# Kernel optimization log

Measured on AMD Instinct MI355X. Metric: run time of the kernel, lower is better.

Reference implementation:

```python
import jax, jax.numpy as jnp
import numpy as np

# --- constants matching the torch module's default-camera / material / light setup ---
IMAGE_SIZE = 128
SCALE = 1.0
FOCAL = 12.0
R_MAT = jnp.array([[-1.0, 0.0, 0.0], [0.0, 1.0, 0.0], [0.0, 0.0, -1.0]], dtype=jnp.float32)
T_VEC = jnp.array([0.0, 0.0, 2.0 * SCALE], dtype=jnp.float32)
CAM_POS = jnp.array([0.0, 0.0, 2.0 * SCALE], dtype=jnp.float32)  # camera center in world coords
LIGHT_LOC = jnp.array([0.0, 1.0, 3.0], dtype=jnp.float32)
AMB_L, DIFF_L, SPEC_L = 0.5, 0.3, 0.2          # PointLights defaults
MAT_AMB, MAT_DIFF, MAT_SPEC = 1.0, 1.0, 0.6    # Materials(specular_color=0.6)
SHININESS = 10.0
TEXEL = jnp.array([142.0, 179.0, 247.0], dtype=jnp.float32) / 255.0  # uniform vertex color
BG = 1.0  # BlendParams background
EPS = 1e-8


def _normalize(v):
    return v / (jnp.linalg.norm(v, axis=-1, keepdims=True) + EPS)


def _render_one(verts, faces):
    """verts: [V,3] world space; faces: [F,3] int. Returns ([3,H,W] rgb*255, [1,H,W] alpha)."""
    H = W = IMAGE_SIZE
    # world -> view (PyTorch3D row-vector convention: x_view = x @ R + T)
    view = verts @ R_MAT + T_VEC              # [V,3]
    z = view[:, 2]                            # [V] view-space depth (>0 in front)
    ndc = FOCAL * view[:, :2] / z[:, None]    # [V,2] perspective projection to NDC
    tri = ndc[faces]                          # [F,3,2]
    tz = z[faces]                             # [F,3]

    # pixel centers in NDC (PyTorch3D: +x left, +y up)
    xs = 1.0 - (2.0 * jnp.arange(W) + 1.0) / W
    ys = 1.0 - (2.0 * jnp.arange(H) + 1.0) / H
    gy, gx = jnp.meshgrid(ys, xs, indexing='ij')
    px = gx.reshape(-1).astype(jnp.float32)   # [P]
    py = gy.reshape(-1).astype(jnp.float32)   # [P]

    v0, v1, v2 = tri[:, 0], tri[:, 1], tri[:, 2]   # [F,2]

    def edge(a, b):  # signed area cross(b-a, p-a) for all pixels -> [P,F]
        return ((b[:, 0] - a[:, 0])[None] * (py[:, None] - a[:, 1][None])
                - (b[:, 1] - a[:, 1])[None] * (px[:, None] - a[:, 0][None]))

    area = ((v1[:, 0] - v0[:, 0]) * (v2[:, 1] - v0[:, 1])
            - (v1[:, 1] - v0[:, 1]) * (v2[:, 0] - v0[:, 0]))   # [F]
    area_safe = jnp.where(jnp.abs(area) < EPS, EPS, area)
    b0 = edge(v1, v2) / area_safe             # [P,F]
    b1 = edge(v2, v0) / area_safe
    b2 = 1.0 - b0 - b1
    inside = (b0 >= 0) & (b1 >= 0) & (b2 >= 0) & (jnp.abs(area) > EPS)[None]

    # perspective-correct interpolated depth: z_pix = 1 / sum_i(b_i / z_i)
    S = b0 / tz[:, 0] + b1 / tz[:, 1] + b2 / tz[:, 2]
    depth = jnp.where(inside & (S > EPS), 1.0 / jnp.maximum(S, EPS), jnp.inf)
    fidx = jnp.argmin(depth, axis=1)          # [P] z-buffer winner (faces_per_pixel=1)
    hit = jnp.isfinite(jnp.min(depth, axis=1))

    # --- recompute barycentrics only for the winning face per pixel (cheap, [P]) ---
    f = faces[fidx]                           # [P,3]
    tv = ndc[f]                               # [P,3,2]
    tzp = z[f]                                # [P,3]
    a0, a1, a2 = tv[:, 0], tv[:, 1], tv[:, 2]

    def edge_p(a, b):
        return (b[:, 0] - a[:, 0]) * (py - a[:, 1]) - (b[:, 1] - a[:, 1]) * (px - a[:, 0])

    ar = (a1[:, 0] - a0[:, 0]) * (a2[:, 1] - a0[:, 1]) - (a1[:, 1] - a0[:, 1]) * (a2[:, 0] - a0[:, 0])
    ar = jnp.where(jnp.abs(ar) < EPS, EPS, ar)
    bb0 = edge_p(a1, a2) / ar
    bb1 = edge_p(a2, a0) / ar
    bb2 = 1.0 - bb0 - bb1
    w = jnp.stack([bb0 / tzp[:, 0], bb1 / tzp[:, 1], bb2 / tzp[:, 2]], axis=-1)
    pc = w / (jnp.sum(w, axis=-1, keepdims=True) + EPS)   # [P,3] perspective-correct barycentrics

    # --- vertex normals (world space) ---
    fv = verts[faces]                         # [F,3,3]
    fn = jnp.cross(fv[:, 1] - fv[:, 0], fv[:, 2] - fv[:, 0])  # [F,3]
    vn = (jnp.zeros_like(verts)
          .at[faces[:, 0]].add(fn)
          .at[faces[:, 1]].add(fn)
          .at[faces[:, 2]].add(fn))
    vn = _normalize(vn)

    # --- interpolate position/normal, Phong shade ---
    pos = jnp.einsum('pk,pkd->pd', pc, verts[f])   # [P,3]
    nrm = _normalize(jnp.einsum('pk,pkd->pd', pc, vn[f]))
    l = _normalize(LIGHT_LOC - pos)
    vdir = _normalize(CAM_POS - pos)
    ndl = jax.nn.relu(jnp.sum(nrm * l, axis=-1))          # [P]
    refl = 2.0 * jnp.sum(nrm * l, axis=-1, keepdims=True) * nrm - l
    spec_cos = jax.nn.relu(jnp.sum(refl * vdir, axis=-1))
    ambient = AMB_L * MAT_AMB
    diffuse = DIFF_L * MAT_DIFF * ndl
    specular = SPEC_L * MAT_SPEC * spec_cos ** SHININESS
    color = TEXEL[None] * (ambient + diffuse[:, None]) + specular[:, None]

    rgb = jnp.where(hit[:, None], color, BG)              # hard blend with white bg
    alpha = hit.astype(verts.dtype)
    img = rgb.reshape(H, W, 3).transpose(2, 0, 1) * 255.0  # [3,H,W]
    a = alpha.reshape(1, H, W)
    return img, a


def setup_inputs() -> dict:
    key = jax.random.key(0)
    k1, k2 = jax.random.split(key)
    B, V, F = 2, 1300, 2500
    vertices = jax.random.normal(k1, (B, V, 3), dtype=jnp.float32) * 0.05  # head-scale mesh near origin
    faces = jax.random.randint(k2, (F, 3), 0, V, dtype=jnp.int32)
    return {"vertices": vertices, "faces": faces}


def reference(vertices, faces):
    # ori_size == image_size, so the area-interpolation in the torch module is the identity.
    images, alphas = jax.lax.map(lambda v: _render_one(v, faces), vertices)
    return images, alphas
```

## Files before the change

### kernel.cpp

```cpp
#include <hip/hip_runtime.h>
#include <math.h>

#pragma clang fp contract(off)

#define IMG_H 128
#define IMG_W 128
#define HW (IMG_H * IMG_W)
#define NB 2
#define NV 1300
#define NF 2500
#define EPSF 1e-8f
#define NCHUNK 32
#define CHUNK ((NF + NCHUNK - 1) / NCHUNK)
#define NREG 128
#define NBLK (NREG * NB * NCHUNK)

#define OFF_FACE 31232
#define OFF_DBUF 351488

#define DINIT 0x7F800000FFFFFFFFull

__global__ __launch_bounds__(256) void k_face(const float* __restrict__ verts,
                                              const int* __restrict__ faces,
                                              float* __restrict__ vn,
                                              float4* __restrict__ face) {
    int i = blockIdx.x * 256 + threadIdx.x;
    if (i >= NB * NF) return;
    int b = i / NF;
    int f = i - b * NF;
    int i0 = faces[f * 3 + 0];
    int i1 = faces[f * 3 + 1];
    int i2 = faces[f * 3 + 2];
    const float* wv = verts + (size_t)b * NV * 3;
    float v0x = wv[i0 * 3 + 0], v0y = wv[i0 * 3 + 1], v0z = wv[i0 * 3 + 2];
    float v1x = wv[i1 * 3 + 0], v1y = wv[i1 * 3 + 1], v1z = wv[i1 * 3 + 2];
    float v2x = wv[i2 * 3 + 0], v2y = wv[i2 * 3 + 1], v2z = wv[i2 * 3 + 2];
    float z0 = 2.0f - v0z, z1 = 2.0f - v1z, z2 = 2.0f - v2z;
    float p0x = (12.0f * (-v0x)) / z0, p0y = (12.0f * v0y) / z0;
    float p1x = (12.0f * (-v1x)) / z1, p1y = (12.0f * v1y) / z1;
    float p2x = (12.0f * (-v2x)) / z2, p2y = (12.0f * v2y) / z2;

    float t1 = (p1x - p0x) * (p2y - p0y);
    float t2 = (p1y - p0y) * (p2x - p0x);
    float area = t1 - t2;
    float aabs = fabsf(area);
    float area_safe = (aabs < EPSF) ? EPSF : area;
    bool valid = aabs > EPSF;
    float minx, maxx, miny, maxy;
    if (valid) {
        minx = fminf(p0x, fminf(p1x, p2x)) - 1e-3f;
        maxx = fmaxf(p0x, fmaxf(p1x, p2x)) + 1e-3f;
        miny = fminf(p0y, fminf(p1y, p2y)) - 1e-3f;
        maxy = fmaxf(p0y, fmaxf(p1y, p2y)) + 1e-3f;
    } else {
        minx = 1e30f; maxx = -1e30f; miny = 1e30f; maxy = -1e30f;
    }
    int o = (b * NF + f) * 4;
    face[o + 0] = make_float4(p2x - p1x, p2y - p1y, p1x, p1y);
    face[o + 1] = make_float4(p0x - p2x, p0y - p2y, p2x, p2y);
    face[o + 2] = make_float4(area_safe, z0, z1, z2);
    face[o + 3] = make_float4(minx, maxx, miny, maxy);

    float ax = v1x - v0x, ay = v1y - v0y, az = v1z - v0z;
    float bx = v2x - v0x, by = v2y - v0y, bz = v2z - v0z;
    float fnx = ay * bz - az * by;
    float fny = az * bx - ax * bz;
    float fnz = ax * by - ay * bx;
    float* vnb = vn + (size_t)b * NV * 3;
    atomicAdd(&vnb[i0 * 3 + 0], fnx);
    atomicAdd(&vnb[i0 * 3 + 1], fny);
    atomicAdd(&vnb[i0 * 3 + 2], fnz);
    atomicAdd(&vnb[i1 * 3 + 0], fnx);
    atomicAdd(&vnb[i1 * 3 + 1], fny);
    atomicAdd(&vnb[i1 * 3 + 2], fnz);
    atomicAdd(&vnb[i2 * 3 + 0], fnx);
    atomicAdd(&vnb[i2 * 3 + 1], fny);
    atomicAdd(&vnb[i2 * 3 + 2], fnz);
}

__global__ __launch_bounds__(128) void k_raster(const float4* __restrict__ face,
                                                unsigned long long* __restrict__ dbuf) {
    __shared__ float4 sface[2][CHUNK * 4];
    __shared__ unsigned short sidx[2][CHUNK];

    int bx = blockIdx.x;
    int chunk = bx & (NCHUNK - 1);
    int tmp = bx >> 5;
    int b = tmp & 1;
    int reg = tmp >> 1;
    int r0 = (reg >> 3) * 8;
    int c0 = (reg & 7) * 16;
    int f0 = chunk * CHUNK;
    int nf = NF - f0; if (nf > CHUNK) nf = CHUNK;

    int t = threadIdx.x;
    int wid = t >> 6, lid = t & 63;
    int cw0 = c0 + wid * 8;

    float txhi = 1.0f - (2.0f * (float)cw0 + 1.0f) / 128.0f;
    float txlo = 1.0f - (2.0f * (float)(cw0 + 7) + 1.0f) / 128.0f;
    float tyhi = 1.0f - (2.0f * (float)r0 + 1.0f) / 128.0f;
    float tylo = 1.0f - (2.0f * (float)(r0 + 7) + 1.0f) / 128.0f;

    const float4* fb = face + (size_t)b * NF * 4;

    int cnt = 0;
    for (int base = 0; base < nf; base += 64) {
        int tt = base + lid;
        bool pass = false;
        float4 bb, E0, E1, FD;
        if (tt < nf) {
            bb = fb[(f0 + tt) * 4 + 3];
            pass = (bb.y >= txlo) && (bb.x <= txhi) && (bb.w >= tylo) && (bb.z <= tyhi);
            if (pass) {
                E0 = fb[(f0 + tt) * 4 + 0];
                E1 = fb[(f0 + tt) * 4 + 1];
                FD = fb[(f0 + tt) * 4 + 2];
                float as = FD.x;
                float u0l = E0.x * (tylo - E0.w), u0h = E0.x * (tyhi - E0.w);
                float u0mn = fminf(u0l, u0h), u0mx = fmaxf(u0l, u0h);
                float u1l = E1.x * (tylo - E1.w), u1h = E1.x * (tyhi - E1.w);
                float u1mn = fminf(u1l, u1h), u1mx = fmaxf(u1l, u1h);
                float v0l = E0.y * (txlo - E0.z), v0h = E0.y * (txhi - E0.z);
                float v0mn = fminf(v0l, v0h), v0mx = fmaxf(v0l, v0h);
                float v1l = E1.y * (txlo - E1.z), v1h = E1.y * (txhi - E1.z);
                float v1mn = fminf(v1l, v1h), v1mx = fmaxf(v1l, v1h);
                float e0mx = u0mx - v0mn, e0mn = u0mn - v0mx;
                float e1mx = u1mx - v1mn, e1mn = u1mn - v1mx;
                const float DL = 1e-4f;
                bool ok;
                if (as > 0.0f) {
                    ok = (e0mx >= -DL) && (e1mx >= -DL) && (((as - e0mn) - e1mn) >= -DL);
                } else {
                    ok = (e0mn <= DL) && (e1mn <= DL) && (((as - e0mx) - e1mx) <= DL);
                }
                pass = ok;
            }
        }
        unsigned long long m = __ballot(pass);
        if (pass) {
            int pos = cnt + __popcll(m & ((1ull << lid) - 1ull));
            sface[wid][pos * 4 + 0] = E0;
            sface[wid][pos * 4 + 1] = E1;
            sface[wid][pos * 4 + 2] = FD;
            sface[wid][pos * 4 + 3] = bb;
            sidx[wid][pos] = (unsigned short)tt;
        }
        cnt += __popcll(m);
    }

    int r = r0 + (lid >> 3);
    int c = cw0 + (lid & 7);
    int p = r * IMG_W + c;
    float px = 1.0f - (2.0f * (float)c + 1.0f) / 128.0f;
    float py = 1.0f - (2.0f * (float)r + 1.0f) / 128.0f;

    unsigned long long best = DINIT;
    for (int j = 0; j < cnt; ++j) {
        float4 fbb = sface[wid][j * 4 + 3];
        if (px >= fbb.x && px <= fbb.y && py >= fbb.z && py <= fbb.w) {
            float4 e0v = sface[wid][j * 4 + 0];
            float4 e1v = sface[wid][j * 4 + 1];
            float4 fdv = sface[wid][j * 4 + 2];
            float u1 = e0v.x * (py - e0v.w);
            float u2 = e0v.y * (px - e0v.z);
            float e0 = u1 - u2;
            float u3 = e1v.x * (py - e1v.w);
            float u4 = e1v.y * (px - e1v.z);
            float e1 = u3 - u4;
            float as = fdv.x;
            bool ok = (as > 0.0f) ? (e0 >= 0.0f && e1 >= 0.0f)
                                  : (e0 <= 0.0f && e1 <= 0.0f);
            if (ok) {
                float b0 = e0 / as;
                float b1 = e1 / as;
                float b2 = (1.0f - b0) - b1;
                if (b2 >= 0.0f) {
                    float S = ((b0 / fdv.y) + (b1 / fdv.z)) + (b2 / fdv.w);
                    if (S > EPSF) {
                        float depth = 1.0f / fmaxf(S, EPSF);
                        unsigned long long pk =
                            ((unsigned long long)__float_as_uint(depth) << 32) |
                            (unsigned)(f0 + sidx[wid][j]);
                        if (pk < best) best = pk;
                    }
                }
            }
        }
    }
    dbuf[((size_t)chunk * NB + b) * HW + p] = best;
}

__global__ __launch_bounds__(64) void k_shade(const float* __restrict__ verts,
                                              const int* __restrict__ faces,
                                              const float* __restrict__ vn,
                                              const unsigned long long* __restrict__ dbuf,
                                              float* __restrict__ out) {
    int i = blockIdx.x * 64 + threadIdx.x;
    int b = i >> 14;
    int p = i & (HW - 1);
    unsigned long long pk = DINIT;
    for (int k = 0; k < NCHUNK; ++k) {
        unsigned long long v = dbuf[((size_t)k * NB + b) * HW + p];
        if (v < pk) pk = v;
    }
    unsigned dbits = (unsigned)(pk >> 32);
    bool hit = dbits < 0x7F800000u;
    float cr = 255.0f, cg = 255.0f, cb = 255.0f, alpha = 0.0f;
    if (hit) {
        alpha = 1.0f;
        int f = (int)(unsigned)(pk & 0xFFFFFFFFull);
        int row = p >> 7;
        int col = p & 127;
        float px = 1.0f - (2.0f * (float)col + 1.0f) / 128.0f;
        float py = 1.0f - (2.0f * (float)row + 1.0f) / 128.0f;
        int i0 = faces[f * 3 + 0];
        int i1 = faces[f * 3 + 1];
        int i2 = faces[f * 3 + 2];
        const float* wv = verts + (size_t)b * NV * 3;
        float v0x = wv[i0 * 3 + 0], v0y = wv[i0 * 3 + 1], v0z = wv[i0 * 3 + 2];
        float v1x = wv[i1 * 3 + 0], v1y = wv[i1 * 3 + 1], v1z = wv[i1 * 3 + 2];
        float v2x = wv[i2 * 3 + 0], v2y = wv[i2 * 3 + 1], v2z = wv[i2 * 3 + 2];
        float z0 = 2.0f - v0z, z1 = 2.0f - v1z, z2 = 2.0f - v2z;
        float a0x = (12.0f * (-v0x)) / z0, a0y = (12.0f * v0y) / z0;
        float a1x = (12.0f * (-v1x)) / z1, a1y = (12.0f * v1y) / z1;
        float a2x = (12.0f * (-v2x)) / z2, a2y = (12.0f * v2y) / z2;

        float t1 = (a1x - a0x) * (a2y - a0y);
        float t2 = (a1y - a0y) * (a2x - a0x);
        float ar = t1 - t2;
        ar = (fabsf(ar) < EPSF) ? EPSF : ar;
        float u1 = (a2x - a1x) * (py - a1y);
        float u2 = (a2y - a1y) * (px - a1x);
        float bb0 = (u1 - u2) / ar;
        float u3 = (a0x - a2x) * (py - a2y);
        float u4 = (a0y - a2y) * (px - a2x);
        float bb1 = (u3 - u4) / ar;
        float bb2 = (1.0f - bb0) - bb1;
        float w0 = bb0 / z0;
        float w1 = bb1 / z1;
        float w2 = bb2 / z2;
        float denom = ((w0 + w1) + w2) + EPSF;
        float pc0 = w0 / denom;
        float pc1 = w1 / denom;
        float pc2 = w2 / denom;

        float posx = (pc0 * v0x + pc1 * v1x) + pc2 * v2x;
        float posy = (pc0 * v0y + pc1 * v1y) + pc2 * v2y;
        float posz = (pc0 * v0z + pc1 * v1z) + pc2 * v2z;

        const float* vnb = vn + (size_t)b * NV * 3;
        float n0x = vnb[i0 * 3 + 0], n0y = vnb[i0 * 3 + 1], n0z = vnb[i0 * 3 + 2];
        float n1x = vnb[i1 * 3 + 0], n1y = vnb[i1 * 3 + 1], n1z = vnb[i1 * 3 + 2];
        float n2x = vnb[i2 * 3 + 0], n2y = vnb[i2 * 3 + 1], n2z = vnb[i2 * 3 + 2];
        float in0 = 1.0f / (sqrtf(n0x * n0x + n0y * n0y + n0z * n0z) + EPSF);
        float in1 = 1.0f / (sqrtf(n1x * n1x + n1y * n1y + n1z * n1z) + EPSF);
        float in2 = 1.0f / (sqrtf(n2x * n2x + n2y * n2y + n2z * n2z) + EPSF);
        n0x *= in0; n0y *= in0; n0z *= in0;
        n1x *= in1; n1y *= in1; n1z *= in1;
        n2x *= in2; n2y *= in2; n2z *= in2;
        float nx = (pc0 * n0x + pc1 * n1x) + pc2 * n2x;
        float ny = (pc0 * n0y + pc1 * n1y) + pc2 * n2y;
        float nz = (pc0 * n0z + pc1 * n1z) + pc2 * n2z;
        float inn = 1.0f / (sqrtf(nx * nx + ny * ny + nz * nz) + EPSF);
        nx *= inn; ny *= inn; nz *= inn;

        float lx = 0.0f - posx, ly = 1.0f - posy, lz = 3.0f - posz;
        float iln = 1.0f / (sqrtf(lx * lx + ly * ly + lz * lz) + EPSF);
        lx *= iln; ly *= iln; lz *= iln;
        float vx = 0.0f - posx, vy = 0.0f - posy, vz = 2.0f - posz;
        float ivn = 1.0f / (sqrtf(vx * vx + vy * vy + vz * vz) + EPSF);
        vx *= ivn; vy *= ivn; vz *= ivn;

        float ndl = nx * lx + ny * ly + nz * lz;
        float ndlr = fmaxf(ndl, 0.0f);
        float rx = 2.0f * ndl * nx - lx;
        float ry = 2.0f * ndl * ny - ly;
        float rz = 2.0f * ndl * nz - lz;
        float sc = fmaxf(rx * vx + ry * vy + rz * vz, 0.0f);
        float spec = 0.2f * 0.6f * powf(sc, 10.0f);
        float shade = 0.5f * 1.0f + 0.3f * 1.0f * ndlr;
        cr = ((142.0f / 255.0f) * shade + spec) * 255.0f;
        cg = ((179.0f / 255.0f) * shade + spec) * 255.0f;
        cb = ((247.0f / 255.0f) * shade + spec) * 255.0f;
    }
    float* img = out + (size_t)b * 3 * HW;
    img[0 * HW + p] = cr;
    img[1 * HW + p] = cg;
    img[2 * HW + p] = cb;
    out[(size_t)NB * 3 * HW + (size_t)b * HW + p] = alpha;
}

extern "C" void kernel_launch(void* const* d_in, const int* in_sizes, int n_in,
                              void* d_out, int out_size, void* d_ws, size_t ws_size,
                              hipStream_t stream) {
    const float* verts = (const float*)d_in[0];
    const int* faces = (const int*)d_in[1];
    char* ws = (char*)d_ws;
    float* vn = (float*)(ws + 0);
    float4* face = (float4*)(ws + OFF_FACE);
    unsigned long long* dbuf = (unsigned long long*)(ws + OFF_DBUF);
    float* out = (float*)d_out;

    hipMemsetAsync(vn, 0, NB * NV * 3 * sizeof(float), stream);
    k_face<<<(NB * NF + 255) / 256, 256, 0, stream>>>(verts, faces, vn, face);
    k_raster<<<NBLK, 128, 0, stream>>>(face, dbuf);
    k_shade<<<(NB * HW) / 64, 64, 0, stream>>>(verts, faces, vn, dbuf, out);
}
```

Before: 101.8 us.

## Use SoA face layout and readlane broadcast instead of LDS compaction in raster

Face records are stored structure-of-arrays so each of the four float4 fields is read with coalesced loads. The raster kernel no longer compacts surviving faces into shared memory and re-reads them. Instead it walks the ballot mask and broadcasts each surviving face's data from its lane with readlane, then tests all pixels against it. This removes the LDS traffic and the two-phase structure. In exchange all four float4s are now loaded unconditionally, and each survivor costs sixteen scalar readlanes.

Result: slower. 103.9 us (+2.1%).

```diff
diff --git a/kernel.cpp b/kernel.cpp
--- a/kernel.cpp
+++ b/kernel.cpp
@@ -19,6 +19,10 @@
 #define OFF_DBUF 351488
 
 #define DINIT 0x7F800000FFFFFFFFull
+
+__device__ __forceinline__ float bcastf(float v, int s) {
+    return __int_as_float(__builtin_amdgcn_readlane(__float_as_int(v), s));
+}
 
 __global__ __launch_bounds__(256) void k_face(const float* __restrict__ verts,
                                               const int* __restrict__ faces,
@@ -55,11 +59,11 @@
     } else {
         minx = 1e30f; maxx = -1e30f; miny = 1e30f; maxy = -1e30f;
     }
-    int o = (b * NF + f) * 4;
-    face[o + 0] = make_float4(p2x - p1x, p2y - p1y, p1x, p1y);
-    face[o + 1] = make_float4(p0x - p2x, p0y - p2y, p2x, p2y);
-    face[o + 2] = make_float4(area_safe, z0, z1, z2);
-    face[o + 3] = make_float4(minx, maxx, miny, maxy);
+    int o = b * NF + f;
+    face[0 * NB * NF + o] = make_float4(p2x - p1x, p2y - p1y, p1x, p1y);
+    face[1 * NB * NF + o] = make_float4(p0x - p2x, p0y - p2y, p2x, p2y);
+    face[2 * NB * NF + o] = make_float4(area_safe, z0, z1, z2);
+    face[3 * NB * NF + o] = make_float4(minx, maxx, miny, maxy);
 
     float ax = v1x - v0x, ay = v1y - v0y, az = v1z - v0z;
     float bx = v2x - v0x, by = v2y - v0y, bz = v2z - v0z;
@@ -80,9 +84,6 @@
 
 __global__ __launch_bounds__(128) void k_raster(const float4* __restrict__ face,
                                                 unsigned long long* __restrict__ dbuf) {
-    __shared__ float4 sface[2][CHUNK * 4];
-    __shared__ unsigned short sidx[2][CHUNK];
-
     int bx = blockIdx.x;
     int chunk = bx & (NCHUNK - 1);
     int tmp = bx >> 5;
@@ -102,20 +103,30 @@
     float tyhi = 1.0f - (2.0f * (float)r0 + 1.0f) / 128.0f;
     float tylo = 1.0f - (2.0f * (float)(r0 + 7) + 1.0f) / 128.0f;
 
-    const float4* fb = face + (size_t)b * NF * 4;
-
-    int cnt = 0;
+    const float4* pE0 = face + (size_t)(0 * NB + b) * NF + f0;
+    const float4* pE1 = face + (size_t)(1 * NB + b) * NF + f0;
+    const float4* pFD = face + (size_t)(2 * NB + b) * NF + f0;
+    const float4* pBB = face + (size_t)(3 * NB + b) * NF + f0;
+
+    int r = r0 + (lid >> 3);
+    int c = cw0 + (lid & 7);
+    int p = r * IMG_W + c;
+    float px = 1.0f - (2.0f * (float)c + 1.0f) / 128.0f;
+    float py = 1.0f - (2.0f * (float)r + 1.0f) / 128.0f;
+
+    unsigned long long best = DINIT;
+
     for (int base = 0; base < nf; base += 64) {
         int tt = base + lid;
+        int fi = (tt < nf) ? tt : (nf - 1);
+        float4 bb = pBB[fi];
+        float4 E0 = pE0[fi];
+        float4 E1 = pE1[fi];
+        float4 FD = pFD[fi];
         bool pass = false;
-        float4 bb, E0, E1, FD;
         if (tt < nf) {
-            bb = fb[(f0 + tt) * 4 + 3];
             pass = (bb.y >= txlo) && (bb.x <= txhi) && (bb.w >= tylo) && (bb.z <= tyhi);
             if (pass) {
-                E0 = fb[(f0 + tt) * 4 + 0];
-                E1 = fb[(f0 + tt) * 4 + 1];
-                FD = fb[(f0 + tt) * 4 + 2];
                 float as = FD.x;
                 float u0l = E0.x * (tylo - E0.w), u0h = E0.x * (tyhi - E0.w);
                 float u0mn = fminf(u0l, u0h), u0mx = fmaxf(u0l, u0h);
@@ -128,61 +139,47 @@
                 float e0mx = u0mx - v0mn, e0mn = u0mn - v0mx;
                 float e1mx = u1mx - v1mn, e1mn = u1mn - v1mx;
                 const float DL = 1e-4f;
-                bool ok;
                 if (as > 0.0f) {
-                    ok = (e0mx >= -DL) && (e1mx >= -DL) && (((as - e0mn) - e1mn) >= -DL);
+                    pass = (e0mx >= -DL) && (e1mx >= -DL) && (((as - e0mn) - e1mn) >= -DL);
                 } else {
-                    ok = (e0mn <= DL) && (e1mn <= DL) && (((as - e0mx) - e1mx) <= DL);
+                    pass = (e0mn <= DL) && (e1mn <= DL) && (((as - e0mx) - e1mx) <= DL);
                 }
-                pass = ok;
             }
         }
         unsigned long long m = __ballot(pass);
-        if (pass) {
-            int pos = cnt + __popcll(m & ((1ull << lid) - 1ull));
-            sface[wid][pos * 4 + 0] = E0;
-            sface[wid][pos * 4 + 1] = E1;
-            sface[wid][pos * 4 + 2] = FD;
-            sface[wid][pos * 4 + 3] = bb;
-            sidx[wid][pos] = (unsigned short)tt;
-        }
-        cnt += __popcll(m);
-    }
-
-    int r = r0 + (lid >> 3);
-    int c = cw0 + (lid & 7);
-    int p = r * IMG_W + c;
-    float px = 1.0f - (2.0f * (float)c + 1.0f) / 128.0f;
-    float py = 1.0f - (2.0f * (float)r + 1.0f) / 128.0f;
-
-    unsigned long long best = DINIT;
-    for (int j = 0; j < cnt; ++j) {
-        float4 fbb = sface[wid][j * 4 + 3];
-        if (px >= fbb.x && px <= fbb.y && py >= fbb.z && py <= fbb.w) {
-            float4 e0v = sface[wid][j * 4 + 0];
-            float4 e1v = sface[wid][j * 4 + 1];
-            float4 fdv = sface[wid][j * 4 + 2];
-            float u1 = e0v.x * (py - e0v.w);
-            float u2 = e0v.y * (px - e0v.z);
-            float e0 = u1 - u2;
-            float u3 = e1v.x * (py - e1v.w);
-            float u4 = e1v.y * (px - e1v.z);
-            float e1 = u3 - u4;
-            float as = fdv.x;
-            bool ok = (as > 0.0f) ? (e0 >= 0.0f && e1 >= 0.0f)
-                                  : (e0 <= 0.0f && e1 <= 0.0f);
-            if (ok) {
-                float b0 = e0 / as;
-                float b1 = e1 / as;
-                float b2 = (1.0f - b0) - b1;
-                if (b2 >= 0.0f) {
-                    float S = ((b0 / fdv.y) + (b1 / fdv.z)) + (b2 / fdv.w);
-                    if (S > EPSF) {
-                        float depth = 1.0f / fmaxf(S, EPSF);
-                        unsigned long long pk =
-                            ((unsigned long long)__float_as_uint(depth) << 32) |
-                            (unsigned)(f0 + sidx[wid][j]);
-                        if (pk < best) best = pk;
+        while (m) {
+            int s = (int)__builtin_ctzll(m);
+            m &= m - 1;
+            float bmnx = bcastf(bb.x, s), bmxx = bcastf(bb.y, s);
+            float bmny = bcastf(bb.z, s), bmxy = bcastf(bb.w, s);
+            if (px >= bmnx && px <= bmxx && py >= bmny && py <= bmxy) {
+                float e0x = bcastf(E0.x, s), e0y = bcastf(E0.y, s);
+                float e0z = bcastf(E0.z, s), e0w = bcastf(E0.w, s);
+                float e1x = bcastf(E1.x, s), e1y = bcastf(E1.y, s);
+                float e1z = bcastf(E1.z, s), e1w = bcastf(E1.w, s);
+                float as  = bcastf(FD.x, s), fz0 = bcastf(FD.y, s);
+                float fz1 = bcastf(FD.z, s), fz2 = bcastf(FD.w, s);
+                float u1 = e0x * (py - e0w);
+                float u2 = e0y * (px - e0z);
+                float e0 = u1 - u2;
+                float u3 = e1x * (py - e1w);
+                float u4 = e1y * (px - e1z);
+                float e1 = u3 - u4;
+                bool ok = (as > 0.0f) ? (e0 >= 0.0f && e1 >= 0.0f)
+                                      : (e0 <= 0.0f && e1 <= 0.0f);
+                if (ok) {
+                    float b0 = e0 / as;
+                    float b1 = e1 / as;
+                    float b2 = (1.0f - b0) - b1;
+                    if (b2 >= 0.0f) {
+                        float S = ((b0 / fz0) + (b1 / fz1)) + (b2 / fz2);
+                        if (S > EPSF) {
+                            float depth = 1.0f / fmaxf(S, EPSF);
+                            unsigned long long pk =
+                                ((unsigned long long)__float_as_uint(depth) << 32) |
+                                (unsigned)(f0 + base + s);
+                            if (pk < best) best = pk;
+                        }
                     }
                 }
             }
```
